# Kernel optimization log

Hardware: AMD Instinct MI355X
Metric: run time of the kernel (lower is better)

Reference implementation:

```python
import jax, jax.numpy as jnp
import numpy as np

ATTN_SCALE = 0.12  # attn_args.attn_scale (constant hyperparameter)
EPS = 1e-6         # F.rms_norm eps
GATE_IN = 12       # attn_gate input features (x[..., :12])


def rms_norm(x):
    return x * jax.lax.rsqrt(jnp.mean(x * x, axis=-1, keepdims=True) + EPS)


def rotary(x, cos, sin):
    # x: [B,T,H,D]; cos/sin: [T,D//2]
    x1, x2 = jnp.split(x, 2, axis=-1)
    c = cos[None, :, None, :]
    s = sin[None, :, None, :]
    return jnp.concatenate([x1 * c + x2 * s, -x1 * s + x2 * c], axis=-1)


def setup_inputs() -> dict:
    key = jax.random.key(0)
    ks = jax.random.split(key, 5)
    B, T, D, H, HD = 1, 2048, 1024, 8, 128
    std = 0.5 * D ** -0.5
    x = jax.random.normal(ks[0], (B, T, D), jnp.float32)
    qkvo_w = jax.random.normal(ks[1], (4, D, D), jnp.float32) * std
    gate_w = jax.random.normal(ks[2], (H, GATE_IN), jnp.float32) * 0.02
    ve = jax.random.normal(ks[3], (B, T, H, HD), jnp.float32)
    sa_lambdas = jax.random.uniform(ks[4], (2,), jnp.float32, 0.3, 0.7)
    half = HD // 2
    inv_freq = 1.0 / (10000.0 ** (jnp.arange(half, dtype=jnp.float32) / half))
    ang = jnp.arange(T, dtype=jnp.float32)[:, None] * inv_freq[None, :]
    return dict(x=x, qkvo_w=qkvo_w, gate_w=gate_w, ve=ve,
                sa_lambdas=sa_lambdas, cos=jnp.cos(ang), sin=jnp.sin(ang))


def reference(x, qkvo_w, gate_w, ve, sa_lambdas, cos, sin):
    B, T, D = x.shape
    H = gate_w.shape[0]
    HD = D // H
    # fused QKV projection: rows of qkvo_w[:3] are [q; k; v]
    w_qkv = qkvo_w[:3].reshape(3 * D, D)           # [3D, D]
    qkv = jnp.einsum('btd,ed->bte', x, w_qkv)      # [B,T,3D]
    qkv = qkv.reshape(B, T, 3, H, HD)
    q, k, v = qkv[:, :, 0], qkv[:, :, 1], qkv[:, :, 2]
    # RMSNorm + RoPE on q, k
    q = rotary(rms_norm(q), cos, sin)
    k = rotary(rms_norm(k), cos, sin)
    # value-residual mixing
    v = sa_lambdas[0] * v + sa_lambdas[1] * ve
    # causal SDPA with custom scale
    scores = jnp.einsum('bqhd,bkhd->bhqk', q, k) * ATTN_SCALE
    causal = jnp.tril(jnp.ones((T, T), dtype=bool))
    scores = jnp.where(causal[None, None], scores, jnp.finfo(scores.dtype).min)
    p = jax.nn.softmax(scores, axis=-1)
    y = jnp.einsum('bhqk,bkhd->bqhd', p, v)        # [B,T,H,HD]
    # per-head sigmoid gate from the first 12 channels of x
    gate = jax.nn.sigmoid(jnp.einsum('bti,hi->bth', x[..., :GATE_IN], gate_w))
    y = y * gate[..., None]
    # output projection (qkvo_w[3]): F.linear -> y @ W_o^T
    out = jnp.einsum('bti,oi->bto', y.reshape(B, T, H * HD), qkvo_w[3])
    return out
```

## Files before the change

kernel.cpp:

```cpp
#include <hip/hip_runtime.h>
#include <stdint.h>

typedef unsigned short u16;
typedef unsigned int u32;

typedef __bf16 bfx8 __attribute__((ext_vector_type(8)));
typedef float fx4 __attribute__((ext_vector_type(4)));
typedef float fx16 __attribute__((ext_vector_type(16)));
typedef u16 u16x4 __attribute__((ext_vector_type(4)));
typedef u16 u16x8 __attribute__((ext_vector_type(8)));

#define GAS __attribute__((address_space(1)))
#define LAS __attribute__((address_space(3)))

__device__ __forceinline__ void gload16(const void* g, void* l) {
  __builtin_amdgcn_global_load_lds((GAS void*)g, (LAS void*)l, 16, 0, 0);
}

__device__ __forceinline__ u16 f2bf(float f) {
  union { float f; u32 u; } v; v.f = f;
  u32 r = v.u + 0x7fffu + ((v.u >> 16) & 1u);
  return (u16)(r >> 16);
}
__device__ __forceinline__ float bf2f(u16 u) {
  union { u32 u; float f; } v; v.u = ((u32)u) << 16;
  return v.f;
}

__device__ __forceinline__ int segF(int qb) { return (qb * qb + 2 * qb + (qb & 1)) >> 2; }

__global__ __launch_bounds__(256) void k_cvt(const float* __restrict__ src, u16* __restrict__ dst, int n) {
  int i = (blockIdx.x * 256 + threadIdx.x) * 8;
  if (i >= n) return;
  const float4* s = (const float4*)(src + i);
  float4 a = s[0], b = s[1];
  u16x8 o;
  o[0] = f2bf(a.x); o[1] = f2bf(a.y); o[2] = f2bf(a.z); o[3] = f2bf(a.w);
  o[4] = f2bf(b.x); o[5] = f2bf(b.y); o[6] = f2bf(b.z); o[7] = f2bf(b.w);
  *(u16x8*)(dst + i) = o;
}

__global__ __launch_bounds__(256) void k_gemm_out(const u16* __restrict__ A, const u16* __restrict__ B,
                                                  float* __restrict__ C, int M, int N, int K) {
  __shared__ char sm[16384];
  const int tid = threadIdx.x;
  const int l = tid & 63, w = tid >> 6;
  const int li = l & 15, lg = l >> 4;
  const int bid = (blockIdx.x & 7) * 64 + (blockIdx.x >> 3);
  const int nbm = M >> 6;
  const int bm = bid % nbm, bn = bid / nbm;

  const u16* gsrc[4];
#pragma unroll
  for (int i = 0; i < 4; ++i) {
    int b = i * 4096 + tid * 16;
    int row, ch;
    const u16* mat;
    if (b < 8192) { row = b >> 7; mat = A + (size_t)(bm * 64 + row) * K; }
    else          { int bb = b - 8192; row = bb >> 7; mat = B + (size_t)(bn * 64 + row) * K; }
    ch = ((b >> 4) & 7) ^ (row & 7);
    gsrc[i] = mat + ch * 8;
  }

  fx4 acc[4];
#pragma unroll
  for (int jj = 0; jj < 4; ++jj)
#pragma unroll
    for (int r = 0; r < 4; ++r) acc[jj][r] = 0.f;

  for (int k0 = 0; k0 < K; k0 += 64) {
    __syncthreads();
#pragma unroll
    for (int i = 0; i < 4; ++i) gload16(gsrc[i] + k0, sm + i * 4096 + w * 1024);
    __syncthreads();
#pragma unroll
    for (int kk = 0; kk < 2; ++kk) {
      int rowa = w * 16 + li;
      bfx8 af = *(const bfx8*)(sm + rowa * 128 + (((kk * 4 + lg)) ^ (rowa & 7)) * 16);
#pragma unroll
      for (int nf = 0; nf < 4; ++nf) {
        int rowb = nf * 16 + li;
        bfx8 bfr = *(const bfx8*)(sm + 8192 + rowb * 128 + ((kk * 4 + lg) ^ (rowb & 7)) * 16);
        acc[nf] = __builtin_amdgcn_mfma_f32_16x16x32_bf16(af, bfr, acc[nf], 0, 0, 0);
      }
    }
  }
#pragma unroll
  for (int nf = 0; nf < 4; ++nf)
#pragma unroll
    for (int r = 0; r < 4; ++r) {
      int row = bm * 64 + w * 16 + lg * 4 + r;
      int col = bn * 64 + nf * 16 + li;
      C[(size_t)row * N + col] = acc[nf][r];
    }
}

__global__ __launch_bounds__(256) void k_gemm_qkv(const u16* __restrict__ A, const u16* __restrict__ B,
                                                  u16* __restrict__ qkv, u16* __restrict__ vt,
                                                  const float* __restrict__ ve, const float* __restrict__ lam,
                                                  const float* __restrict__ cosp, const float* __restrict__ sinp) {
  __shared__ char sm[24576];
  const int tid = threadIdx.x;
  const int l = tid & 63, w = tid >> 6;
  const int li = l & 15, lg = l >> 4;
  const int bid = (blockIdx.x & 7) * 96 + (blockIdx.x >> 3);
  const int bm = bid & 31, bn = bid >> 5;
  const int K = 1024;

  const u16* gsrc[6];
#pragma unroll
  for (int i = 0; i < 6; ++i) {
    int b = i * 4096 + tid * 16;
    int row, ch;
    const u16* mat;
    if (b < 8192) { row = b >> 7; mat = A + (size_t)(bm * 64 + row) * K; }
    else          { int bb = b - 8192; row = bb >> 7; mat = B + (size_t)(bn * 128 + row) * K; }
    ch = ((b >> 4) & 7) ^ (row & 7);
    gsrc[i] = mat + ch * 8;
  }

  fx4 acc[8];
#pragma unroll
  for (int jj = 0; jj < 8; ++jj)
#pragma unroll
    for (int r = 0; r < 4; ++r) acc[jj][r] = 0.f;

  for (int k0 = 0; k0 < K; k0 += 64) {
    __syncthreads();
#pragma unroll
    for (int i = 0; i < 6; ++i) gload16(gsrc[i] + k0, sm + i * 4096 + w * 1024);
    __syncthreads();
#pragma unroll
    for (int kk = 0; kk < 2; ++kk) {
      int rowa = w * 16 + li;
      bfx8 af = *(const bfx8*)(sm + rowa * 128 + ((kk * 4 + lg) ^ (rowa & 7)) * 16);
#pragma unroll
      for (int nf = 0; nf < 8; ++nf) {
        int rowb = nf * 16 + li;
        bfx8 bfr = *(const bfx8*)(sm + 8192 + rowb * 128 + ((kk * 4 + lg) ^ (rowb & 7)) * 16);
        acc[nf] = __builtin_amdgcn_mfma_f32_16x16x32_bf16(af, bfr, acc[nf], 0, 0, 0);
      }
    }
  }

  const int s = bn >> 3, h = bn & 7;
  if (s < 2) {
#pragma unroll
    for (int r = 0; r < 4; ++r) {
      int t = bm * 64 + w * 16 + lg * 4 + r;
      float ss = 0.f;
#pragma unroll
      for (int nf = 0; nf < 8; ++nf) ss += acc[nf][r] * acc[nf][r];
      ss += __shfl_xor(ss, 1); ss += __shfl_xor(ss, 2);
      ss += __shfl_xor(ss, 4); ss += __shfl_xor(ss, 8);
      float rn = rsqrtf(ss * (1.f / 128.f) + 1e-6f);
      u16* qp = qkv + (size_t)t * 3072 + s * 1024 + h * 128;
#pragma unroll
      for (int nf = 0; nf < 4; ++nf) {
        int dp = nf * 16 + li;
        float c = cosp[(size_t)t * 64 + dp];
        float sn = sinp[(size_t)t * 64 + dp];
        float x1 = acc[nf][r] * rn, x2 = acc[nf + 4][r] * rn;
        qp[dp] = f2bf(x1 * c + x2 * sn);
        qp[dp + 64] = f2bf(-x1 * sn + x2 * c);
      }
    }
  } else {
    const float l0 = lam[0], l1 = lam[1];
    int tb = bm * 64 + w * 16 + lg * 4;
#pragma unroll
    for (int nf = 0; nf < 8; ++nf) {
      int d = nf * 16 + li;
      u16x4 o;
#pragma unroll
      for (int r = 0; r < 4; ++r)
        o[r] = f2bf(l0 * acc[nf][r] + l1 * ve[(size_t)(tb + r) * 1024 + h * 128 + d]);
      *(u16x4*)(vt + (size_t)h * 262144 + (size_t)d * 2048 + tb) = o;
    }
  }
}

__global__ __launch_bounds__(256) void k_attn2(const u16* __restrict__ qkv, const u16* __restrict__ vt,
                                               u16* __restrict__ part, float* __restrict__ ml) {
  __shared__ char sm[32768];
  const int bid = (blockIdx.x & 7) * 72 + (blockIdx.x >> 3);
  const int h = bid / 72;
  const int r72 = bid % 72;
  int qb = 15;
  while (segF(qb) > r72) --qb;
  const int s = r72 - segF(qb);
  const int q0 = qb * 128;
  const int seg0 = s * 256;
  const int seg_len = min(256, (qb + 1) * 128 - seg0);
  const int nkt = seg_len >> 5;

  const int tid = threadIdx.x;
  const int l = tid & 63, w = tid >> 6;
  const int li = l & 31, hi = l >> 5;
  const int qrow = q0 + w * 32 + li;
  const int wqmax = q0 + w * 32 + 31;
  const int wqmin = q0 + w * 32;

  bfx8 Q[8];
  {
    const u16* qp = qkv + (size_t)qrow * 3072 + h * 128 + hi * 8;
#pragma unroll
    for (int c = 0; c < 8; ++c) Q[c] = *(const bfx8*)(qp + c * 16);
  }

  const u16* kbase = qkv + 1024 + h * 128;
  const u16* vbase = vt + (size_t)h * 262144;

  auto STAGE = [&](int kt, int buf) {
    const int kabs = seg0 + kt * 32;
    char* dst = sm + buf * 16384;
#pragma unroll
    for (int i = 0; i < 2; ++i) {
      int j = w * 2 + i;
      int row = j * 4 + (l >> 4);
      int ch = (l & 15) ^ (row & 7);
      gload16(kbase + (size_t)(kabs + row) * 3072 + ch * 8, dst + j * 1024);
    }
#pragma unroll
    for (int i = 0; i < 2; ++i) {
      int j = w * 2 + i;
      int d = (j & 1) * 64 + l;
      int slot = j >> 1;
      gload16(vbase + (size_t)d * 2048 + kabs + slot * 8, dst + 8192 + j * 1024);
    }
  };

  fx16 Y[4];
#pragma unroll
  for (int d = 0; d < 4; ++d)
#pragma unroll
    for (int r = 0; r < 16; ++r) Y[d][r] = 0.f;
  float m_run = -1e30f, l_run = 0.f;

  STAGE(0, 0);
  __syncthreads();
  int cur = 0;

  for (int kt = 0; kt < nkt; ++kt) {
    if (kt + 1 < nkt) STAGE(kt + 1, cur ^ 1);
    const int k0 = seg0 + kt * 32;
    if (k0 <= wqmax) {
      const char* kb = sm + cur * 16384;
      const char* vb = kb + 8192;
      fx16 S;
#pragma unroll
      for (int r = 0; r < 16; ++r) S[r] = 0.f;
#pragma unroll
      for (int c = 0; c < 8; ++c) {
        int ch = (c * 2 + hi) ^ (li & 7);
        bfx8 kf = *(const bfx8*)(kb + li * 256 + ch * 16);
        S = __builtin_amdgcn_mfma_f32_32x32x16_bf16(kf, Q[c], S, 0, 0, 0);
      }
      const bool nomask = (k0 + 31 <= wqmin);
      float p[16];
      float mt = -1e30f;
#pragma unroll
      for (int r = 0; r < 16; ++r) {
        int kk = (r & 3) + 8 * (r >> 2) + 4 * hi;
        float sv = (nomask || (k0 + kk <= qrow)) ? S[r] * 0.12f : -1e30f;
        p[r] = sv;
        mt = fmaxf(mt, sv);
      }
      mt = fmaxf(mt, __shfl_xor(mt, 32));
      float mnew = fmaxf(m_run, mt);
      float alpha = __expf(m_run - mnew);
      float ssum = 0.f;
#pragma unroll
      for (int r = 0; r < 16; ++r) { float e = __expf(p[r] - mnew); p[r] = e; ssum += e; }
      ssum += __shfl_xor(ssum, 32);
      l_run = l_run * alpha + ssum;
      m_run = mnew;
#pragma unroll
      for (int d = 0; d < 4; ++d)
#pragma unroll
        for (int r = 0; r < 16; ++r) Y[d][r] *= alpha;
      u32 pk[8], pks[8];
#pragma unroll
      for (int i = 0; i < 8; ++i) pk[i] = (u32)f2bf(p[2 * i]) | ((u32)f2bf(p[2 * i + 1]) << 16);
#pragma unroll
      for (int i = 0; i < 8; ++i) pks[i] = (u32)__shfl_xor((int)pk[i], 32);
      union { u32 u[4]; bfx8 v; } P0, P1;
      if (hi == 0) {
        P0.u[0] = pk[0];  P0.u[1] = pk[1];  P0.u[2] = pks[0]; P0.u[3] = pks[1];
        P1.u[0] = pk[4];  P1.u[1] = pk[5];  P1.u[2] = pks[4]; P1.u[3] = pks[5];
      } else {
        P0.u[0] = pks[2]; P0.u[1] = pks[3]; P0.u[2] = pk[2];  P0.u[3] = pk[3];
        P1.u[0] = pks[6]; P1.u[1] = pks[7]; P1.u[2] = pk[6];  P1.u[3] = pk[7];
      }
#pragma unroll
      for (int db = 0; db < 4; ++db) {
        int dd = db * 32 + li;
        bfx8 v0 = *(const bfx8*)(vb + hi * 2048 + dd * 16);
        bfx8 v1 = *(const bfx8*)(vb + (2 + hi) * 2048 + dd * 16);
        Y[db] = __builtin_amdgcn_mfma_f32_32x32x16_bf16(v0, P0.v, Y[db], 0, 0, 0);
        Y[db] = __builtin_amdgcn_mfma_f32_32x32x16_bf16(v1, P1.v, Y[db], 0, 0, 0);
      }
    }
    __syncthreads();
    cur ^= 1;
  }

  if (hi == 0) {
    ml[(size_t)bid * 256 + (w * 32 + li) * 2 + 0] = m_run;
    ml[(size_t)bid * 256 + (w * 32 + li) * 2 + 1] = l_run;
  }
  float* Yl = (float*)(sm + w * 8192);
  u16* pdst = part + (size_t)bid * 16384;
#pragma unroll
  for (int P = 0; P < 2; ++P) {
    asm volatile("" ::: "memory");
#pragma unroll
    for (int dh = 0; dh < 2; ++dh) {
      int db = P * 2 + dh;
#pragma unroll
      for (int r = 0; r < 16; ++r) {
        int dloc = dh * 32 + (r & 3) + 8 * (r >> 2) + 4 * hi;
        Yl[li * 64 + (dloc ^ ((li & 7) << 2))] = Y[db][r];
      }
    }
    asm volatile("" ::: "memory");
    int rr = l >> 1, c0 = (l & 1) * 32, sx = (rr & 7) << 2;
#pragma unroll
    for (int j = 0; j < 8; ++j) {
      float4 v = *(const float4*)(Yl + rr * 64 + ((c0 + j * 4) ^ sx));
      u16x4 o;
      o[0] = f2bf(v.x); o[1] = f2bf(v.y); o[2] = f2bf(v.z); o[3] = f2bf(v.w);
      *(u16x4*)(pdst + (w * 32 + rr) * 128 + P * 64 + c0 + j * 4) = o;
    }
  }
}

__global__ __launch_bounds__(256) void k_comb(const u16* __restrict__ part, const float* __restrict__ ml,
                                              const float* __restrict__ x, const float* __restrict__ gw,
                                              u16* __restrict__ y) {
  const int b = blockIdx.x;
  const int h = b >> 4, qb = b & 15;
  const int nseg = (qb + 2) >> 1;
  const int slot0 = h * 72 + segF(qb);
  const int t = threadIdx.x;
  const int r = t >> 1, hf = (t & 1) * 64;
  const int q = qb * 128 + r;

  float ms[8], ls[8];
  float M = -1e30f;
#pragma unroll
  for (int s = 0; s < 8; ++s) {
    if (s < nseg) {
      ms[s] = ml[(size_t)(slot0 + s) * 256 + r * 2 + 0];
      ls[s] = ml[(size_t)(slot0 + s) * 256 + r * 2 + 1];
      M = fmaxf(M, ms[s]);
    }
  }
  float wt[8];
  float L = 0.f;
#pragma unroll
  for (int s = 0; s < 8; ++s) {
    if (s < nseg) { wt[s] = __expf(ms[s] - M); L += wt[s] * ls[s]; }
  }
  float accv[64];
#pragma unroll
  for (int j = 0; j < 64; ++j) accv[j] = 0.f;
#pragma unroll
  for (int s = 0; s < 8; ++s) {
    if (s < nseg) {
      const u16x8* P = (const u16x8*)(part + (size_t)(slot0 + s) * 16384 + r * 128 + hf);
      float ws_ = wt[s];
#pragma unroll
      for (int j = 0; j < 8; ++j) {
        u16x8 v = P[j];
#pragma unroll
        for (int e = 0; e < 8; ++e) accv[j * 8 + e] += ws_ * bf2f(v[e]);
      }
    }
  }
  float dot = 0.f;
#pragma unroll
  for (int i = 0; i < 12; ++i) dot += x[(size_t)q * 1024 + i] * gw[h * 12 + i];
  float gt_ = 1.f / (1.f + __expf(-dot));
  float sc = gt_ / L;
  u16* yp = y + (size_t)q * 1024 + h * 128 + hf;
#pragma unroll
  for (int j = 0; j < 8; ++j) {
    u16x8 o;
#pragma unroll
    for (int e = 0; e < 8; ++e) o[e] = f2bf(accv[j * 8 + e] * sc);
    *(u16x8*)(yp + j * 8) = o;
  }
}

extern "C" void kernel_launch(void* const* d_in, const int* in_sizes, int n_in,
                              void* d_out, int out_size, void* d_ws, size_t ws_size,
                              hipStream_t stream) {
  const float* x = (const float*)d_in[0];
  const float* qkvo_w = (const float*)d_in[1];
  const float* gate_w = (const float*)d_in[2];
  const float* ve = (const float*)d_in[3];
  const float* lam = (const float*)d_in[4];
  const float* cosp = (const float*)d_in[5];
  const float* sinp = (const float*)d_in[6];
  float* out = (float*)d_out;

  u16* wb  = (u16*)d_ws;
  u16* xb  = wb + 4u * 1024 * 1024;
  u16* qkv = xb + 2u * 1024 * 1024;
  u16* vt  = qkv + 6u * 1024 * 1024;
  u16* y   = vt + 2u * 1024 * 1024;
  u16* part = y + 2u * 1024 * 1024;
  float* ml = (float*)(part + (size_t)576 * 16384);

  k_cvt<<<dim3(2048), dim3(256), 0, stream>>>(qkvo_w, wb, 4 * 1024 * 1024);
  k_cvt<<<dim3(1024), dim3(256), 0, stream>>>(x, xb, 2 * 1024 * 1024);
  k_gemm_qkv<<<dim3(32 * 24), dim3(256), 0, stream>>>(xb, wb, qkv, vt, ve, lam, cosp, sinp);
  k_attn2<<<dim3(576), dim3(256), 0, stream>>>(qkv, vt, part, ml);
  k_comb<<<dim3(128), dim3(256), 0, stream>>>(part, ml, x, gate_w, y);
  k_gemm_out<<<dim3(32 * 16), dim3(256), 0, stream>>>(y, wb + 3u * 1024 * 1024, out, 2048, 1024, 1024);
}
```

Baseline: 101.2 us.

## Load K/V fragments directly from global memory instead of staging through LDS

The double-buffered LDS staging of K and V tiles (global_load_lds plus a __syncthreads per key tile) is replaced by per-wave direct global loads of K and V fragments into registers. Each wave also loops only up to its own causal limit instead of the block-wide tile count. This removes the block barriers and LDS traffic and lets waves run independently. In exchange, the four waves in a block each fetch the same K/V data from global memory or cache, and there is no explicit prefetch to hide load latency.

```diff
diff --git a/kernel.cpp b/kernel.cpp
--- a/kernel.cpp
+++ b/kernel.cpp
@@ -208,27 +208,8 @@
     for (int c = 0; c < 8; ++c) Q[c] = *(const bfx8*)(qp + c * 16);
   }
 
-  const u16* kbase = qkv + 1024 + h * 128;
-  const u16* vbase = vt + (size_t)h * 262144;
-
-  auto STAGE = [&](int kt, int buf) {
-    const int kabs = seg0 + kt * 32;
-    char* dst = sm + buf * 16384;
-#pragma unroll
-    for (int i = 0; i < 2; ++i) {
-      int j = w * 2 + i;
-      int row = j * 4 + (l >> 4);
-      int ch = (l & 15) ^ (row & 7);
-      gload16(kbase + (size_t)(kabs + row) * 3072 + ch * 8, dst + j * 1024);
-    }
-#pragma unroll
-    for (int i = 0; i < 2; ++i) {
-      int j = w * 2 + i;
-      int d = (j & 1) * 64 + l;
-      int slot = j >> 1;
-      gload16(vbase + (size_t)d * 2048 + kabs + slot * 8, dst + 8192 + j * 1024);
-    }
-  };
+  const u16* krow = qkv + 1024 + h * 128 + (size_t)(seg0 + li) * 3072 + hi * 8;
+  const u16* vseg = vt + (size_t)h * 262144 + seg0;
 
   fx16 Y[4];
 #pragma unroll
@@ -237,72 +218,66 @@
     for (int r = 0; r < 16; ++r) Y[d][r] = 0.f;
   float m_run = -1e30f, l_run = 0.f;
 
-  STAGE(0, 0);
-  __syncthreads();
-  int cur = 0;
-
-  for (int kt = 0; kt < nkt; ++kt) {
-    if (kt + 1 < nkt) STAGE(kt + 1, cur ^ 1);
+  const int mkt = min(nkt, ((wqmax - seg0) >> 5) + 1);
+
+  for (int kt = 0; kt < mkt; ++kt) {
     const int k0 = seg0 + kt * 32;
-    if (k0 <= wqmax) {
-      const char* kb = sm + cur * 16384;
-      const char* vb = kb + 8192;
-      fx16 S;
-#pragma unroll
-      for (int r = 0; r < 16; ++r) S[r] = 0.f;
-#pragma unroll
-      for (int c = 0; c < 8; ++c) {
-        int ch = (c * 2 + hi) ^ (li & 7);
-        bfx8 kf = *(const bfx8*)(kb + li * 256 + ch * 16);
-        S = __builtin_amdgcn_mfma_f32_32x32x16_bf16(kf, Q[c], S, 0, 0, 0);
-      }
-      const bool nomask = (k0 + 31 <= wqmin);
-      float p[16];
-      float mt = -1e30f;
-#pragma unroll
-      for (int r = 0; r < 16; ++r) {
-        int kk = (r & 3) + 8 * (r >> 2) + 4 * hi;
-        float sv = (nomask || (k0 + kk <= qrow)) ? S[r] * 0.12f : -1e30f;
-        p[r] = sv;
-        mt = fmaxf(mt, sv);
-      }
-      mt = fmaxf(mt, __shfl_xor(mt, 32));
-      float mnew = fmaxf(m_run, mt);
-      float alpha = __expf(m_run - mnew);
-      float ssum = 0.f;
-#pragma unroll
-      for (int r = 0; r < 16; ++r) { float e = __expf(p[r] - mnew); p[r] = e; ssum += e; }
-      ssum += __shfl_xor(ssum, 32);
-      l_run = l_run * alpha + ssum;
-      m_run = mnew;
-#pragma unroll
-      for (int d = 0; d < 4; ++d)
-#pragma unroll
-        for (int r = 0; r < 16; ++r) Y[d][r] *= alpha;
-      u32 pk[8], pks[8];
-#pragma unroll
-      for (int i = 0; i < 8; ++i) pk[i] = (u32)f2bf(p[2 * i]) | ((u32)f2bf(p[2 * i + 1]) << 16);
-#pragma unroll
-      for (int i = 0; i < 8; ++i) pks[i] = (u32)__shfl_xor((int)pk[i], 32);
-      union { u32 u[4]; bfx8 v; } P0, P1;
-      if (hi == 0) {
-        P0.u[0] = pk[0];  P0.u[1] = pk[1];  P0.u[2] = pks[0]; P0.u[3] = pks[1];
-        P1.u[0] = pk[4];  P1.u[1] = pk[5];  P1.u[2] = pks[4]; P1.u[3] = pks[5];
-      } else {
-        P0.u[0] = pks[2]; P0.u[1] = pks[3]; P0.u[2] = pk[2];  P0.u[3] = pk[3];
-        P1.u[0] = pks[6]; P1.u[1] = pks[7]; P1.u[2] = pk[6];  P1.u[3] = pk[7];
-      }
-#pragma unroll
-      for (int db = 0; db < 4; ++db) {
-        int dd = db * 32 + li;
-        bfx8 v0 = *(const bfx8*)(vb + hi * 2048 + dd * 16);
-        bfx8 v1 = *(const bfx8*)(vb + (2 + hi) * 2048 + dd * 16);
-        Y[db] = __builtin_amdgcn_mfma_f32_32x32x16_bf16(v0, P0.v, Y[db], 0, 0, 0);
-        Y[db] = __builtin_amdgcn_mfma_f32_32x32x16_bf16(v1, P1.v, Y[db], 0, 0, 0);
-      }
-    }
-    __syncthreads();
-    cur ^= 1;
+    bfx8 kf[8];
+#pragma unroll
+    for (int c = 0; c < 8; ++c)
+      kf[c] = *(const bfx8*)(krow + (size_t)kt * (32 * 3072) + c * 16);
+    fx16 S;
+#pragma unroll
+    for (int r = 0; r < 16; ++r) S[r] = 0.f;
+#pragma unroll
+    for (int c = 0; c < 8; ++c)
+      S = __builtin_amdgcn_mfma_f32_32x32x16_bf16(kf[c], Q[c], S, 0, 0, 0);
+
+    const bool nomask = (k0 + 31 <= wqmin);
+    float p[16];
+    float mt = -1e30f;
+#pragma unroll
+    for (int r = 0; r < 16; ++r) {
+      int kk = (r & 3) + 8 * (r >> 2) + 4 * hi;
+      float sv = (nomask || (k0 + kk <= qrow)) ? S[r] * 0.12f : -1e30f;
+      p[r] = sv;
+      mt = fmaxf(mt, sv);
+    }
+    mt = fmaxf(mt, __shfl_xor(mt, 32));
+    float mnew = fmaxf(m_run, mt);
+    float alpha = __expf(m_run - mnew);
+    float ssum = 0.f;
+#pragma unroll
+    for (int r = 0; r < 16; ++r) { float e = __expf(p[r] - mnew); p[r] = e; ssum += e; }
+    ssum += __shfl_xor(ssum, 32);
+    l_run = l_run * alpha + ssum;
+    m_run = mnew;
+#pragma unroll
+    for (int d = 0; d < 4; ++d)
+#pragma unroll
+      for (int r = 0; r < 16; ++r) Y[d][r] *= alpha;
+    u32 pk[8], pks[8];
+#pragma unroll
+    for (int i = 0; i < 8; ++i) pk[i] = (u32)f2bf(p[2 * i]) | ((u32)f2bf(p[2 * i + 1]) << 16);
+#pragma unroll
+    for (int i = 0; i < 8; ++i) pks[i] = (u32)__shfl_xor((int)pk[i], 32);
+    union { u32 u[4]; bfx8 v; } P0, P1;
+    if (hi == 0) {
+      P0.u[0] = pk[0];  P0.u[1] = pk[1];  P0.u[2] = pks[0]; P0.u[3] = pks[1];
+      P1.u[0] = pk[4];  P1.u[1] = pk[5];  P1.u[2] = pks[4]; P1.u[3] = pks[5];
+    } else {
+      P0.u[0] = pks[2]; P0.u[1] = pks[3]; P0.u[2] = pk[2];  P0.u[3] = pk[3];
+      P1.u[0] = pks[6]; P1.u[1] = pks[7]; P1.u[2] = pk[6];  P1.u[3] = pk[7];
+    }
+#pragma unroll
+    for (int db = 0; db < 4; ++db) {
+      int dd = db * 32 + li;
+      const u16* vrow = vseg + (size_t)dd * 2048 + kt * 32;
+      bfx8 v0 = *(const bfx8*)(vrow + hi * 8);
+      bfx8 v1 = *(const bfx8*)(vrow + (2 + hi) * 8);
+      Y[db] = __builtin_amdgcn_mfma_f32_32x32x16_bf16(v0, P0.v, Y[db], 0, 0, 0);
+      Y[db] = __builtin_amdgcn_mfma_f32_32x32x16_bf16(v1, P1.v, Y[db], 0, 0, 0);
+    }
   }
 
   if (hi == 0) {
```

Result: slower. 116.2 us (+14.8%).

## Store K and V in pre-swizzled tile-contiguous layout for attention staging

Applied to the files above, without the earlier changes.

The QKV GEMM epilogue now writes Q to its own buffer, K into per-head 32-token tiles with the LDS XOR swizzle already applied, and V into matching tile-contiguous blocks. The attention kernel then stages each K/V tile with fully contiguous 16-byte global-to-LDS loads instead of strided row gathers. This is meant to cut scattered memory traffic and address arithmetic in the attention kernel. The cost is scattered 2-byte stores for K in the GEMM epilogue.

```diff
diff --git a/kernel.cpp b/kernel.cpp
--- a/kernel.cpp
+++ b/kernel.cpp
@@ -96,7 +96,8 @@
 }
 
 __global__ __launch_bounds__(256) void k_gemm_qkv(const u16* __restrict__ A, const u16* __restrict__ B,
-                                                  u16* __restrict__ qkv, u16* __restrict__ vt,
+                                                  u16* __restrict__ qb2, u16* __restrict__ kt2,
+                                                  u16* __restrict__ vt2,
                                                   const float* __restrict__ ve, const float* __restrict__ lam,
                                                   const float* __restrict__ cosp, const float* __restrict__ sinp) {
   __shared__ char sm[24576];
@@ -154,20 +155,30 @@
       ss += __shfl_xor(ss, 1); ss += __shfl_xor(ss, 2);
       ss += __shfl_xor(ss, 4); ss += __shfl_xor(ss, 8);
       float rn = rsqrtf(ss * (1.f / 128.f) + 1e-6f);
-      u16* qp = qkv + (size_t)t * 3072 + s * 1024 + h * 128;
 #pragma unroll
       for (int nf = 0; nf < 4; ++nf) {
         int dp = nf * 16 + li;
         float c = cosp[(size_t)t * 64 + dp];
         float sn = sinp[(size_t)t * 64 + dp];
         float x1 = acc[nf][r] * rn, x2 = acc[nf + 4][r] * rn;
-        qp[dp] = f2bf(x1 * c + x2 * sn);
-        qp[dp + 64] = f2bf(-x1 * sn + x2 * c);
+        u16 o1 = f2bf(x1 * c + x2 * sn);
+        u16 o2 = f2bf(-x1 * sn + x2 * c);
+        if (s == 0) {
+          u16* qp = qb2 + (size_t)t * 1024 + h * 128;
+          qp[dp] = o1;
+          qp[dp + 64] = o2;
+        } else {
+          u16* kp = kt2 + (size_t)h * 262144 + (size_t)(t >> 5) * 4096 + (t & 31) * 128;
+          int dq = dp + 64;
+          kp[(((dp >> 3) ^ (t & 7)) << 3) | (dp & 7)] = o1;
+          kp[(((dq >> 3) ^ (t & 7)) << 3) | (dq & 7)] = o2;
+        }
       }
     }
   } else {
     const float l0 = lam[0], l1 = lam[1];
     int tb = bm * 64 + w * 16 + lg * 4;
+    u16* vbase = vt2 + (size_t)h * 262144 + (size_t)(tb >> 5) * 4096 + ((tb & 31) >> 3) * 1024 + (tb & 7);
 #pragma unroll
     for (int nf = 0; nf < 8; ++nf) {
       int d = nf * 16 + li;
@@ -175,12 +186,13 @@
 #pragma unroll
       for (int r = 0; r < 4; ++r)
         o[r] = f2bf(l0 * acc[nf][r] + l1 * ve[(size_t)(tb + r) * 1024 + h * 128 + d]);
-      *(u16x4*)(vt + (size_t)h * 262144 + (size_t)d * 2048 + tb) = o;
-    }
-  }
-}
-
-__global__ __launch_bounds__(256) void k_attn2(const u16* __restrict__ qkv, const u16* __restrict__ vt,
+      *(u16x4*)(vbase + d * 8) = o;
+    }
+  }
+}
+
+__global__ __launch_bounds__(256) void k_attn2(const u16* __restrict__ qb2, const u16* __restrict__ kt2,
+                                               const u16* __restrict__ vt2,
                                                u16* __restrict__ part, float* __restrict__ ml) {
   __shared__ char sm[32768];
   const int bid = (blockIdx.x & 7) * 72 + (blockIdx.x >> 3);
@@ -203,30 +215,23 @@
 
   bfx8 Q[8];
   {
-    const u16* qp = qkv + (size_t)qrow * 3072 + h * 128 + hi * 8;
+    const u16* qp = qb2 + (size_t)qrow * 1024 + h * 128 + hi * 8;
 #pragma unroll
     for (int c = 0; c < 8; ++c) Q[c] = *(const bfx8*)(qp + c * 16);
   }
 
-  const u16* kbase = qkv + 1024 + h * 128;
-  const u16* vbase = vt + (size_t)h * 262144;
+  const u16* ktile = kt2 + (size_t)h * 262144 + (size_t)(seg0 >> 5) * 4096;
+  const u16* vtile = vt2 + (size_t)h * 262144 + (size_t)(seg0 >> 5) * 4096;
 
   auto STAGE = [&](int kt, int buf) {
-    const int kabs = seg0 + kt * 32;
     char* dst = sm + buf * 16384;
+    const u16* ks = ktile + (size_t)kt * 4096;
+    const u16* vs = vtile + (size_t)kt * 4096;
 #pragma unroll
     for (int i = 0; i < 2; ++i) {
       int j = w * 2 + i;
-      int row = j * 4 + (l >> 4);
-      int ch = (l & 15) ^ (row & 7);
-      gload16(kbase + (size_t)(kabs + row) * 3072 + ch * 8, dst + j * 1024);
-    }
-#pragma unroll
-    for (int i = 0; i < 2; ++i) {
-      int j = w * 2 + i;
-      int d = (j & 1) * 64 + l;
-      int slot = j >> 1;
-      gload16(vbase + (size_t)d * 2048 + kabs + slot * 8, dst + 8192 + j * 1024);
+      gload16(ks + j * 512 + l * 8, dst + j * 1024);
+      gload16(vs + j * 512 + l * 8, dst + 8192 + j * 1024);
     }
   };
 
@@ -407,16 +412,17 @@
 
   u16* wb  = (u16*)d_ws;
   u16* xb  = wb + 4u * 1024 * 1024;
-  u16* qkv = xb + 2u * 1024 * 1024;
-  u16* vt  = qkv + 6u * 1024 * 1024;
-  u16* y   = vt + 2u * 1024 * 1024;
+  u16* qb2 = xb + 2u * 1024 * 1024;
+  u16* kt2 = qb2 + 2u * 1024 * 1024;
+  u16* vt2 = kt2 + 2u * 1024 * 1024;
+  u16* y   = vt2 + 2u * 1024 * 1024;
   u16* part = y + 2u * 1024 * 1024;
   float* ml = (float*)(part + (size_t)576 * 16384);
 
   k_cvt<<<dim3(2048), dim3(256), 0, stream>>>(qkvo_w, wb, 4 * 1024 * 1024);
   k_cvt<<<dim3(1024), dim3(256), 0, stream>>>(x, xb, 2 * 1024 * 1024);
-  k_gemm_qkv<<<dim3(32 * 24), dim3(256), 0, stream>>>(xb, wb, qkv, vt, ve, lam, cosp, sinp);
-  k_attn2<<<dim3(576), dim3(256), 0, stream>>>(qkv, vt, part, ml);
+  k_gemm_qkv<<<dim3(32 * 24), dim3(256), 0, stream>>>(xb, wb, qb2, kt2, vt2, ve, lam, cosp, sinp);
+  k_attn2<<<dim3(576), dim3(256), 0, stream>>>(qb2, kt2, vt2, part, ml);
   k_comb<<<dim3(128), dim3(256), 0, stream>>>(part, ml, x, gate_w, y);
   k_gemm_out<<<dim3(32 * 16), dim3(256), 0, stream>>>(y, wb + 3u * 1024 * 1024, out, 2048, 1024, 1024);
 }
```

New measurement: 100.6 us. About the same (-0.6%).
